# Kernel optimization log

Hardware: AMD Instinct MI355X
Metric: run time of the kernel (lower is better)

Reference implementation:

```python
import jax, jax.numpy as jnp
import numpy as np

N_NODES = 200000
N_EDGES = 4000000  # doubled (w2b + b2w), matches edge_weight param size
N_W2B = 2000000


def gcn_conv(x, W, b, src, dst, ew, n):
    # PyG GCNConv with add_self_loops=True, symmetric normalization.
    loop = jnp.arange(n)
    src_sl = jnp.concatenate([src, loop])
    dst_sl = jnp.concatenate([dst, loop])
    w_sl = jnp.concatenate([ew, jnp.ones((n,), ew.dtype)])  # self-loop weight 1
    deg = jax.ops.segment_sum(w_sl, dst_sl, num_segments=n)
    dinv = jnp.where(deg > 0, jax.lax.rsqrt(deg), 0.0)
    norm = dinv[src_sl] * w_sl * dinv[dst_sl]          # [E+N]
    xw = x @ W                                          # [N, out]
    msg = xw[src_sl] * norm[:, None]                    # [E+N, out]
    out = jax.ops.segment_sum(msg, dst_sl, num_segments=n)
    return out + b


def setup_inputs() -> dict:
    key = jax.random.key(0)
    ks = jax.random.split(key, 16)
    h1, h2, h3, h4, out = 8, 16, 32, 4, 3
    inp = 7

    def lin_init(k, fan_in, fan_out):
        bound = 1.0 / np.sqrt(fan_in)
        kw, kb = jax.random.split(k)
        W = jax.random.uniform(kw, (fan_in, fan_out), jnp.float32, -bound, bound)
        b = jax.random.uniform(kb, (fan_out,), jnp.float32, -bound, bound)
        return W, b

    x = jax.random.normal(ks[0], (N_NODES, inp), jnp.float32)
    edge_index = jax.random.randint(ks[1], (2, N_EDGES), 0, N_NODES, jnp.int64)
    w2b = jax.random.randint(ks[2], (2, N_W2B), 0, N_NODES, jnp.int64)
    edge_weight = jnp.ones((N_EDGES,), jnp.float32)  # Parameter init: ones

    W1, b1 = lin_init(ks[3], inp, h1)
    W2, b2 = lin_init(ks[4], h1, h2)
    W3, b3 = lin_init(ks[5], h2, h3)
    Wl1, bl1 = lin_init(ks[6], 2 * h3, h4)
    Wl2, bl2 = lin_init(ks[7], h4, out)

    return dict(x=x, edge_index=edge_index, w2b=w2b, edge_weight=edge_weight,
                W1=W1, b1=b1, W2=W2, b2=b2, W3=W3, b3=b3,
                Wl1=Wl1, bl1=bl1, Wl2=Wl2, bl2=bl2)


def reference(x, edge_index, w2b, edge_weight,
              W1, b1, W2, b2, W3, b3, Wl1, bl1, Wl2, bl2):
    n = x.shape[0]
    src, dst = edge_index[0], edge_index[1]
    ew = jax.nn.sigmoid(edge_weight)
    h = jax.nn.relu(gcn_conv(x, W1, b1, src, dst, ew, n))
    h = jax.nn.relu(gcn_conv(h, W2, b2, src, dst, ew, n))
    h = jax.nn.relu(gcn_conv(h, W3, b3, src, dst, ew, n))
    # fused gather-concat replacing the per-edge python loop
    concat = jnp.concatenate([h[w2b[0]], h[w2b[1]]], axis=-1)  # [E_w2b, 2*h3]
    hidden = concat @ Wl1 + bl1
    edge_pred = hidden @ Wl2 + bl2
    return edge_pred
```

## Files before the change

kernel.cpp:

```cpp
#include <hip/hip_runtime.h>
#include <hip/hip_bf16.h>
#include <hip/hip_fp16.h>


#define NB1 768
#define NPB 256
#define MAXBINS 1024
#define TILE 4096
#define QS 16384.0f
#define QINV (1.0f / 16384.0f)

typedef _Float16 h2 __attribute__((ext_vector_type(2)));
typedef _Float16 h4 __attribute__((ext_vector_type(4)));
typedef _Float16 h8 __attribute__((ext_vector_type(8)));

__device__ __forceinline__ float sigmoidf_(float x) {
    return 1.0f / (1.0f + __expf(-x));
}

__global__ void p1a_hist(const int* __restrict__ dst, int* __restrict__ bh,
                         int ne, int nbins, int chunk) {
    __shared__ int h[MAXBINS];
    for (int k = threadIdx.x; k < nbins; k += 256) h[k] = 0;
    __syncthreads();
    int base = blockIdx.x * chunk;
    int end = min(base + chunk, ne);
    for (int e = base + threadIdx.x; e < end; e += 256)
        atomicAdd(&h[dst[e] >> 8], 1);
    __syncthreads();
    for (int k = threadIdx.x; k < nbins; k += 256)
        bh[(size_t)k * NB1 + blockIdx.x] = h[k];
}

__global__ void s1_scan(int* __restrict__ bh, int* __restrict__ bintot) {
    __shared__ int sums[256];
    constexpr int W = NB1 / 256;
    int* row = bh + (size_t)blockIdx.x * NB1;
    int v[W];
    int s = 0;
#pragma unroll
    for (int j = 0; j < W; ++j) { v[j] = row[threadIdx.x * W + j]; s += v[j]; }
    sums[threadIdx.x] = s;
    __syncthreads();
    for (int o = 1; o < 256; o <<= 1) {
        int t = (threadIdx.x >= o) ? sums[threadIdx.x - o] : 0;
        __syncthreads();
        sums[threadIdx.x] += t;
        __syncthreads();
    }
    int excl = sums[threadIdx.x] - s;
#pragma unroll
    for (int j = 0; j < W; ++j) { row[threadIdx.x * W + j] = excl; excl += v[j]; }
    if (threadIdx.x == 255) bintot[blockIdx.x] = sums[255];
}

__global__ void s2_scan(const int* __restrict__ bintot, int* __restrict__ binbase,
                        int nbins, int ne) {
    __shared__ int tmp[1024];
    int tid = threadIdx.x;
    int v = (tid < nbins) ? bintot[tid] : 0;
    tmp[tid] = v;
    __syncthreads();
    for (int o = 1; o < 1024; o <<= 1) {
        int t = (tid >= o) ? tmp[tid - o] : 0;
        __syncthreads();
        tmp[tid] += t;
        __syncthreads();
    }
    if (tid < nbins) binbase[tid] = tmp[tid] - v;
    if (tid == 0) binbase[nbins] = ne;
}

__global__ void p1b_scatter(const int* __restrict__ src, const int* __restrict__ dst,
                            const float* __restrict__ ew, const int* __restrict__ bh,
                            const int* __restrict__ binbase,
                            unsigned* __restrict__ edlo, unsigned char* __restrict__ eddl,
                            int ne, int nbins, int chunk) {
    __shared__ unsigned slo[TILE];
    __shared__ unsigned shi[TILE];
    __shared__ int hist[MAXBINS];
    __shared__ int boff[MAXBINS];
    __shared__ int cur[MAXBINS];
    __shared__ int wsum[4];
    int tid = threadIdx.x;
    int lane = tid & 63, wid = tid >> 6;
    for (int k = tid; k < nbins; k += 256)
        cur[k] = binbase[k] + bh[(size_t)k * NB1 + blockIdx.x];
    int base = blockIdx.x * chunk;
    int endb = min(base + chunk, ne);
    for (int t0 = base; t0 < endb; t0 += TILE) {
        int cnt = min(TILE, endb - t0);
        for (int k = tid; k < nbins; k += 256) hist[k] = 0;
        __syncthreads();
        for (int j = tid; j < cnt; j += 256)
            atomicAdd(&hist[dst[t0 + j] >> 8], 1);
        __syncthreads();
        int w0 = tid * 4;
        int lv[4];
        int ls = 0;
#pragma unroll
        for (int j = 0; j < 4; ++j) {
            lv[j] = (w0 + j < nbins) ? hist[w0 + j] : 0;
            ls += lv[j];
        }
        int s = ls;
        for (int o = 1; o < 64; o <<= 1) {
            int t = __shfl_up(s, o, 64);
            if (lane >= o) s += t;
        }
        if (lane == 63) wsum[wid] = s;
        __syncthreads();
        int wpre = 0;
        for (int w = 0; w < wid; ++w) wpre += wsum[w];
        int excl = wpre + s - ls;
#pragma unroll
        for (int j = 0; j < 4; ++j) {
            if (w0 + j < nbins) { boff[w0 + j] = excl; excl += lv[j]; }
        }
        __syncthreads();
        for (int j = tid; j < cnt; j += 256) {
            int e = t0 + j;
            int d = dst[e];
            int b = d >> 8;
            float w = sigmoidf_(ew[e]);
            int q = (int)fminf(w * QS + 0.5f, 16383.0f);
            unsigned lo = (unsigned)src[e] | ((unsigned)q << 18);
            int p = atomicAdd(&boff[b], 1);
            slo[p] = lo;
            shi[p] = ((unsigned)b << 8) | (unsigned)(d & 255);
        }
        __syncthreads();
        for (int j = tid; j < cnt; j += 256) {
            unsigned hv = shi[j];
            int b = (int)(hv >> 8);
            int g = cur[b] + (j - (boff[b] - hist[b]));
            edlo[g] = slo[j];
            eddl[g] = (unsigned char)(hv & 255u);
        }
        __syncthreads();
        for (int k = tid; k < nbins; k += 256) cur[k] += hist[k];
        __syncthreads();
    }
}

__global__ void p2_build(const unsigned* __restrict__ edlo, const unsigned char* __restrict__ eddl,
                         const int* __restrict__ binbase, unsigned* __restrict__ edata,
                         int* __restrict__ C, float* __restrict__ dinv,
                         const float* __restrict__ x, const float* __restrict__ W1,
                         _Float16* __restrict__ g0, int n, int ne, int nbins) {
    __shared__ int cnt[NPB];
    __shared__ int curs[NPB];
    __shared__ unsigned qsum[NPB];
    __shared__ float Ws[56];
    __shared__ int wsum[4];
    if (threadIdx.x < 56) Ws[threadIdx.x] = W1[threadIdx.x];
    int b = blockIdx.x;
    int E0 = binbase[b], E1 = binbase[b + 1];
    int tid = threadIdx.x;
    int lane = tid & 63, wid = tid >> 6;
    cnt[tid] = 0;
    qsum[tid] = 0;
    __syncthreads();
    for (int k = E0 + tid; k < E1; k += 256)
        atomicAdd(&cnt[(int)eddl[k]], 1);
    __syncthreads();
    int v = cnt[tid];
    int s = v;
    for (int o = 1; o < 64; o <<= 1) {
        int t = __shfl_up(s, o, 64);
        if (lane >= o) s += t;
    }
    if (lane == 63) wsum[wid] = s;
    __syncthreads();
    int wpre = 0;
    for (int w = 0; w < wid; ++w) wpre += wsum[w];
    int excl = wpre + s - v;
    curs[tid] = E0 + excl;
    int node = b * NPB + tid;
    if (node < n) C[node] = E0 + excl;
    if (b == 0 && tid == 0) C[n] = ne;
    __syncthreads();
    for (int k = E0 + tid; k < E1; k += 256) {
        unsigned lo = edlo[k];
        int dl = (int)eddl[k];
        int pos = atomicAdd(&curs[dl], 1);
        edata[pos] = lo;
        atomicAdd(&qsum[dl], lo >> 18);
    }
    __syncthreads();
    if (node < n) {
        float dv = rsqrtf((float)qsum[tid] * QINV + 1.0f);
        dinv[node] = dv;
        float xi[7];
#pragma unroll
        for (int k = 0; k < 7; ++k) xi[k] = x[(size_t)node * 7 + k];
        h8 r;
#pragma unroll
        for (int o = 0; o < 8; ++o) {
            float acc = 0.0f;
#pragma unroll
            for (int k = 0; k < 7; ++k) acc = fmaf(xi[k], Ws[k * 8 + o], acc);
            r[o] = (_Float16)(acc * dv);
        }
        *reinterpret_cast<h8*>(g0 + (size_t)node * 8) = r;
    }
}

__global__ void gather1_kernel(const _Float16* __restrict__ g, const float* __restrict__ dinv,
                               const int* __restrict__ C, const unsigned* __restrict__ edata,
                               const float* __restrict__ b1, _Float16* __restrict__ out, int n) {
    __shared__ float bs[8];
    if (threadIdx.x < 8) bs[threadIdx.x] = b1[threadIdx.x];
    __syncthreads();
    long long t = (long long)blockIdx.x * blockDim.x + threadIdx.x;
    int i = (int)(t >> 3);
    int l8 = (int)(t & 7);
    if (i >= n) return;
    int beg = C[i], end = C[i + 1];
    float acc[8] = {0.f, 0.f, 0.f, 0.f, 0.f, 0.f, 0.f, 0.f};
    if (l8 == 0) {
        h8 r = *reinterpret_cast<const h8*>(g + (size_t)i * 8);
#pragma unroll
        for (int j = 0; j < 8; ++j) acc[j] = (float)r[j];
    }
    int k = beg + l8;
    for (; k + 8 < end; k += 16) {
        unsigned v0 = edata[k];
        unsigned v1 = edata[k + 8];
        h8 r0 = *reinterpret_cast<const h8*>(g + (size_t)(v0 & 0x3FFFFu) * 8);
        h8 r1 = *reinterpret_cast<const h8*>(g + (size_t)(v1 & 0x3FFFFu) * 8);
        float w0 = (float)(v0 >> 18) * QINV;
        float w1 = (float)(v1 >> 18) * QINV;
#pragma unroll
        for (int j = 0; j < 8; ++j) acc[j] = fmaf((float)r0[j], w0, acc[j]);
#pragma unroll
        for (int j = 0; j < 8; ++j) acc[j] = fmaf((float)r1[j], w1, acc[j]);
    }
    if (k < end) {
        unsigned v = edata[k];
        float w = (float)(v >> 18) * QINV;
        h8 r = *reinterpret_cast<const h8*>(g + (size_t)(v & 0x3FFFFu) * 8);
#pragma unroll
        for (int j = 0; j < 8; ++j) acc[j] = fmaf((float)r[j], w, acc[j]);
    }
    bool t4 = (l8 & 4) != 0, t2 = (l8 & 2) != 0, t1 = (l8 & 1) != 0;
    float s4[4];
#pragma unroll
    for (int j = 0; j < 4; ++j) {
        float keep = t4 ? acc[4 + j] : acc[j];
        float send = t4 ? acc[j] : acc[4 + j];
        s4[j] = keep + __shfl_xor(send, 4, 64);
    }
    float s2[2];
#pragma unroll
    for (int j = 0; j < 2; ++j) {
        float keep = t2 ? s4[2 + j] : s4[j];
        float send = t2 ? s4[j] : s4[2 + j];
        s2[j] = keep + __shfl_xor(send, 2, 64);
    }
    float keep = t1 ? s2[1] : s2[0];
    float send = t1 ? s2[0] : s2[1];
    float s = keep + __shfl_xor(send, 1, 64);
    float dv = dinv[i];
    out[(size_t)i * 8 + l8] = (_Float16)(dv * fmaxf(dv * s + bs[l8], 0.0f));
}

__global__ void gather2_kernel(const _Float16* __restrict__ g, const float* __restrict__ dinv,
                               const int* __restrict__ C, const unsigned* __restrict__ edata,
                               const float* __restrict__ W2, const float* __restrict__ b2,
                               _Float16* __restrict__ out, int n) {
    __shared__ float Ws[128];
    __shared__ float bs[16];
    if (threadIdx.x < 128) Ws[threadIdx.x] = W2[threadIdx.x];
    if (threadIdx.x < 16) bs[threadIdx.x] = b2[threadIdx.x];
    __syncthreads();
    long long t = (long long)blockIdx.x * blockDim.x + threadIdx.x;
    int i = (int)(t >> 3);
    int l8 = (int)(t & 7);
    if (i >= n) return;
    int beg = C[i], end = C[i + 1];
    float acc[8] = {0.f, 0.f, 0.f, 0.f, 0.f, 0.f, 0.f, 0.f};
    if (l8 == 0) {
        h8 r = *reinterpret_cast<const h8*>(g + (size_t)i * 8);
#pragma unroll
        for (int j = 0; j < 8; ++j) acc[j] = (float)r[j];
    }
    int k = beg + l8;
    for (; k + 8 < end; k += 16) {
        unsigned v0 = edata[k];
        unsigned v1 = edata[k + 8];
        h8 r0 = *reinterpret_cast<const h8*>(g + (size_t)(v0 & 0x3FFFFu) * 8);
        h8 r1 = *reinterpret_cast<const h8*>(g + (size_t)(v1 & 0x3FFFFu) * 8);
        float w0 = (float)(v0 >> 18) * QINV;
        float w1 = (float)(v1 >> 18) * QINV;
#pragma unroll
        for (int j = 0; j < 8; ++j) acc[j] = fmaf((float)r0[j], w0, acc[j]);
#pragma unroll
        for (int j = 0; j < 8; ++j) acc[j] = fmaf((float)r1[j], w1, acc[j]);
    }
    if (k < end) {
        unsigned v = edata[k];
        float w = (float)(v >> 18) * QINV;
        h8 r = *reinterpret_cast<const h8*>(g + (size_t)(v & 0x3FFFFu) * 8);
#pragma unroll
        for (int j = 0; j < 8; ++j) acc[j] = fmaf((float)r[j], w, acc[j]);
    }
#pragma unroll
    for (int j = 0; j < 8; ++j) {
        acc[j] += __shfl_xor(acc[j], 1, 64);
        acc[j] += __shfl_xor(acc[j], 2, 64);
        acc[j] += __shfl_xor(acc[j], 4, 64);
    }
    float dv = dinv[i];
    float raw[8];
#pragma unroll
    for (int j = 0; j < 8; ++j) raw[j] = acc[j] * dv;
    int o0 = l8 * 2;
    h2 o2;
#pragma unroll
    for (int jo = 0; jo < 2; ++jo) {
        int o = o0 + jo;
        float h = bs[o];
#pragma unroll
        for (int k2 = 0; k2 < 8; ++k2) h = fmaf(raw[k2], Ws[k2 * 16 + o], h);
        o2[jo] = (_Float16)(dv * fmaxf(h, 0.0f));
    }
    *reinterpret_cast<h2*>(out + (size_t)i * 16 + o0) = o2;
}

__global__ void gather3_kernel(const _Float16* __restrict__ g, const float* __restrict__ dinv,
                               const int* __restrict__ C, const unsigned* __restrict__ edata,
                               _Float16* __restrict__ raw3, int n) {
    long long t = (long long)blockIdx.x * blockDim.x + threadIdx.x;
    int i = (int)(t >> 3);
    int l8 = (int)(t & 7);
    if (i >= n) return;
    int beg = C[i], end = C[i + 1];
    float acc[16];
#pragma unroll
    for (int j = 0; j < 16; ++j) acc[j] = 0.0f;
    if (l8 == 0) {
        h8 r0 = *reinterpret_cast<const h8*>(g + (size_t)i * 16);
        h8 r1 = *reinterpret_cast<const h8*>(g + (size_t)i * 16 + 8);
#pragma unroll
        for (int j = 0; j < 8; ++j) { acc[j] = (float)r0[j]; acc[8 + j] = (float)r1[j]; }
    }
    int k = beg + l8;
    for (; k + 8 < end; k += 16) {
        unsigned v0 = edata[k];
        unsigned v1 = edata[k + 8];
        size_t i0 = (size_t)(v0 & 0x3FFFFu) * 16;
        size_t i1 = (size_t)(v1 & 0x3FFFFu) * 16;
        h8 a0 = *reinterpret_cast<const h8*>(g + i0);
        h8 a1 = *reinterpret_cast<const h8*>(g + i0 + 8);
        h8 c0 = *reinterpret_cast<const h8*>(g + i1);
        h8 c1 = *reinterpret_cast<const h8*>(g + i1 + 8);
        float w0 = (float)(v0 >> 18) * QINV;
        float w1 = (float)(v1 >> 18) * QINV;
#pragma unroll
        for (int j = 0; j < 8; ++j) acc[j] = fmaf((float)a0[j], w0, acc[j]);
#pragma unroll
        for (int j = 0; j < 8; ++j) acc[8 + j] = fmaf((float)a1[j], w0, acc[8 + j]);
#pragma unroll
        for (int j = 0; j < 8; ++j) acc[j] = fmaf((float)c0[j], w1, acc[j]);
#pragma unroll
        for (int j = 0; j < 8; ++j) acc[8 + j] = fmaf((float)c1[j], w1, acc[8 + j]);
    }
    if (k < end) {
        unsigned v = edata[k];
        size_t i0 = (size_t)(v & 0x3FFFFu) * 16;
        h8 a0 = *reinterpret_cast<const h8*>(g + i0);
        h8 a1 = *reinterpret_cast<const h8*>(g + i0 + 8);
        float w = (float)(v >> 18) * QINV;
#pragma unroll
        for (int j = 0; j < 8; ++j) acc[j] = fmaf((float)a0[j], w, acc[j]);
#pragma unroll
        for (int j = 0; j < 8; ++j) acc[8 + j] = fmaf((float)a1[j], w, acc[8 + j]);
    }
    bool t4 = (l8 & 4) != 0, t2 = (l8 & 2) != 0, t1 = (l8 & 1) != 0;
    float s8[8];
#pragma unroll
    for (int j = 0; j < 8; ++j) {
        float keep = t4 ? acc[8 + j] : acc[j];
        float send = t4 ? acc[j] : acc[8 + j];
        s8[j] = keep + __shfl_xor(send, 4, 64);
    }
    float s4[4];
#pragma unroll
    for (int j = 0; j < 4; ++j) {
        float keep = t2 ? s8[4 + j] : s8[j];
        float send = t2 ? s8[j] : s8[4 + j];
        s4[j] = keep + __shfl_xor(send, 2, 64);
    }
    float s2[2];
#pragma unroll
    for (int j = 0; j < 2; ++j) {
        float keep = t1 ? s4[2 + j] : s4[j];
        float send = t1 ? s4[j] : s4[2 + j];
        s2[j] = keep + __shfl_xor(send, 1, 64);
    }
    float dv = dinv[i];
    h2 o2;
    o2[0] = (_Float16)(s2[0] * dv);
    o2[1] = (_Float16)(s2[1] * dv);
    *reinterpret_cast<h2*>(raw3 + (size_t)i * 16 + l8 * 2) = o2;
}

__global__ void dense3_kernel(const _Float16* __restrict__ raw3,
                              const float* __restrict__ W3, const float* __restrict__ b3,
                              const float* __restrict__ Wl1, const float* __restrict__ bl1,
                              const float* __restrict__ Wl2, const float* __restrict__ bl2,
                              _Float16* __restrict__ pqh, int n) {
    __shared__ __align__(16) float WsT[512];
    __shared__ float bs[32];
    __shared__ float wfs[192];
    __shared__ float bfs[3];
    for (int t = threadIdx.x; t < 512; t += 256) {
        int k = t >> 5, o = t & 31;
        WsT[o * 16 + k] = W3[t];
    }
    if (threadIdx.x < 32) bs[threadIdx.x] = b3[threadIdx.x];
    if (threadIdx.x < 192) {
        int f = threadIdx.x / 3, j = threadIdx.x % 3;
        float a = 0.0f;
#pragma unroll
        for (int k = 0; k < 4; ++k) a = fmaf(Wl1[f * 4 + k], Wl2[k * 3 + j], a);
        wfs[threadIdx.x] = a;
    }
    if (threadIdx.x < 3) {
        float a = bl2[threadIdx.x];
#pragma unroll
        for (int k = 0; k < 4; ++k) a = fmaf(bl1[k], Wl2[k * 3 + threadIdx.x], a);
        bfs[threadIdx.x] = a;
    }
    __syncthreads();
    int i = blockIdx.x * 256 + threadIdx.x;
    if (i >= n) return;
    h8 r0 = *reinterpret_cast<const h8*>(raw3 + (size_t)i * 16);
    h8 r1 = *reinterpret_cast<const h8*>(raw3 + (size_t)i * 16 + 8);
    float raw[16];
#pragma unroll
    for (int j = 0; j < 8; ++j) { raw[j] = (float)r0[j]; raw[8 + j] = (float)r1[j]; }
    float p0 = bfs[0], p1 = bfs[1], p2 = bfs[2];
    float q0 = 0.0f, q1 = 0.0f, q2 = 0.0f;
#pragma unroll
    for (int o = 0; o < 32; ++o) {
        const float4* w4 = reinterpret_cast<const float4*>(WsT + o * 16);
        float4 wa = w4[0], wb = w4[1], wc = w4[2], wd = w4[3];
        float h = bs[o];
        h = fmaf(raw[0], wa.x, h);  h = fmaf(raw[1], wa.y, h);
        h = fmaf(raw[2], wa.z, h);  h = fmaf(raw[3], wa.w, h);
        h = fmaf(raw[4], wb.x, h);  h = fmaf(raw[5], wb.y, h);
        h = fmaf(raw[6], wb.z, h);  h = fmaf(raw[7], wb.w, h);
        h = fmaf(raw[8], wc.x, h);  h = fmaf(raw[9], wc.y, h);
        h = fmaf(raw[10], wc.z, h); h = fmaf(raw[11], wc.w, h);
        h = fmaf(raw[12], wd.x, h); h = fmaf(raw[13], wd.y, h);
        h = fmaf(raw[14], wd.z, h); h = fmaf(raw[15], wd.w, h);
        h = fmaxf(h, 0.0f);
        p0 = fmaf(h, wfs[o * 3 + 0], p0);
        p1 = fmaf(h, wfs[o * 3 + 1], p1);
        p2 = fmaf(h, wfs[o * 3 + 2], p2);
        q0 = fmaf(h, wfs[(32 + o) * 3 + 0], q0);
        q1 = fmaf(h, wfs[(32 + o) * 3 + 1], q1);
        q2 = fmaf(h, wfs[(32 + o) * 3 + 2], q2);
    }
    h8 o8;
    o8[0] = (_Float16)p0; o8[1] = (_Float16)p1; o8[2] = (_Float16)p2; o8[3] = (_Float16)0.0f;
    o8[4] = (_Float16)q0; o8[5] = (_Float16)q1; o8[6] = (_Float16)q2; o8[7] = (_Float16)0.0f;
    *reinterpret_cast<h8*>(pqh + (size_t)i * 8) = o8;
}

__global__ void head_kernel(const int* __restrict__ w2b, const _Float16* __restrict__ pqh,
                            float* __restrict__ out, int nw) {
    int e = blockIdx.x * blockDim.x + threadIdx.x;
    if (e >= nw) return;
    int a = w2b[e];
    int b = w2b[(size_t)nw + e];
    h4 P = *reinterpret_cast<const h4*>(pqh + (size_t)a * 8);
    h4 Q = *reinterpret_cast<const h4*>(pqh + (size_t)b * 8 + 4);
    out[(size_t)e * 3 + 0] = (float)P[0] + (float)Q[0];
    out[(size_t)e * 3 + 1] = (float)P[1] + (float)Q[1];
    out[(size_t)e * 3 + 2] = (float)P[2] + (float)Q[2];
}

extern "C" void kernel_launch(void* const* d_in, const int* in_sizes, int n_in,
                              void* d_out, int out_size, void* d_ws, size_t ws_size,
                              hipStream_t stream) {
    const float* x   = (const float*)d_in[0];
    const int* eidx  = (const int*)d_in[1];
    const int* w2b   = (const int*)d_in[2];
    const float* ew  = (const float*)d_in[3];
    const float* W1  = (const float*)d_in[4];
    const float* b1  = (const float*)d_in[5];
    const float* W2  = (const float*)d_in[6];
    const float* b2  = (const float*)d_in[7];
    const float* W3  = (const float*)d_in[8];
    const float* b3  = (const float*)d_in[9];
    const float* Wl1 = (const float*)d_in[10];
    const float* bl1 = (const float*)d_in[11];
    const float* Wl2 = (const float*)d_in[12];
    const float* bl2 = (const float*)d_in[13];
    float* out = (float*)d_out;

    const int n  = in_sizes[0] / 7;
    const int ne = in_sizes[1] / 2;
    const int nw = in_sizes[2] / 2;
    const int* src = eidx;
    const int* dst = eidx + ne;

    const int nbins = (n + NPB - 1) / NPB;
    const int chunk = (ne + NB1 - 1) / NB1;

    float*     ws      = (float*)d_ws;
    float*     dinv    = ws;
    int*       C       = (int*)(ws + n);
    unsigned*  edata   = (unsigned*)(ws + 2 * (size_t)n + 16);
    int*       bh      = (int*)(edata + ne);
    int*       bintot  = bh + (size_t)nbins * NB1;
    int*       binbase = bintot + MAXBINS;
    _Float16*  g0      = (_Float16*)(binbase + MAXBINS);
    float*     bregion = (float*)(g0 + (size_t)n * 8);
    unsigned*  edlo    = (unsigned*)bregion;
    unsigned char* eddl = (unsigned char*)(edlo + ne);
    _Float16*  g1      = (_Float16*)bregion;
    _Float16*  g2      = (_Float16*)(bregion + 4 * (size_t)n);
    _Float16*  pqh     = (_Float16*)(bregion + 12 * (size_t)n);
    _Float16*  raw3    = (_Float16*)(bregion + 16 * (size_t)n);

    const int Bl = 256;
    auto blks = [&](long long t) { return (int)((t + Bl - 1) / Bl); };
    const int nb8 = blks((long long)n * 8);

    p1a_hist<<<NB1, Bl, 0, stream>>>(dst, bh, ne, nbins, chunk);
    s1_scan<<<nbins, Bl, 0, stream>>>(bh, bintot);
    s2_scan<<<1, 1024, 0, stream>>>(bintot, binbase, nbins, ne);
    p1b_scatter<<<NB1, Bl, 0, stream>>>(src, dst, ew, bh, binbase, edlo, eddl, ne, nbins, chunk);
    p2_build<<<nbins, Bl, 0, stream>>>(edlo, eddl, binbase, edata, C, dinv, x, W1, g0, n, ne, nbins);

    gather1_kernel<<<nb8, Bl, 0, stream>>>(g0, dinv, C, edata, b1, g1, n);
    gather2_kernel<<<nb8, Bl, 0, stream>>>(g1, dinv, C, edata, W2, b2, g2, n);
    gather3_kernel<<<nb8, Bl, 0, stream>>>(g2, dinv, C, edata, raw3, n);
    dense3_kernel<<<blks(n), Bl, 0, stream>>>(raw3, W3, b3, Wl1, bl1, Wl2, bl2, pqh, n);

    head_kernel<<<blks(nw), Bl, 0, stream>>>(w2b, pqh, out, nw);
}
```

Before: 365.0 us.

## Replace binned two-pass CSR sort with global-atomic degree count and scatter

```diff
diff --git a/kernel.cpp b/kernel.cpp
--- a/kernel.cpp
+++ b/kernel.cpp
@@ -3,10 +3,8 @@
 #include <hip/hip_fp16.h>
 
 
-#define NB1 768
 #define NPB 256
 #define MAXBINS 1024
-#define TILE 4096
 #define QS 16384.0f
 #define QINV (1.0f / 16384.0f)
 
@@ -18,40 +16,25 @@
     return 1.0f / (1.0f + __expf(-x));
 }
 
-__global__ void p1a_hist(const int* __restrict__ dst, int* __restrict__ bh,
-                         int ne, int nbins, int chunk) {
-    __shared__ int h[MAXBINS];
-    for (int k = threadIdx.x; k < nbins; k += 256) h[k] = 0;
-    __syncthreads();
-    int base = blockIdx.x * chunk;
-    int end = min(base + chunk, ne);
-    for (int e = base + threadIdx.x; e < end; e += 256)
-        atomicAdd(&h[dst[e] >> 8], 1);
-    __syncthreads();
-    for (int k = threadIdx.x; k < nbins; k += 256)
-        bh[(size_t)k * NB1 + blockIdx.x] = h[k];
-}
-
-__global__ void s1_scan(int* __restrict__ bh, int* __restrict__ bintot) {
-    __shared__ int sums[256];
-    constexpr int W = NB1 / 256;
-    int* row = bh + (size_t)blockIdx.x * NB1;
-    int v[W];
-    int s = 0;
-#pragma unroll
-    for (int j = 0; j < W; ++j) { v[j] = row[threadIdx.x * W + j]; s += v[j]; }
-    sums[threadIdx.x] = s;
-    __syncthreads();
-    for (int o = 1; o < 256; o <<= 1) {
-        int t = (threadIdx.x >= o) ? sums[threadIdx.x - o] : 0;
-        __syncthreads();
-        sums[threadIdx.x] += t;
-        __syncthreads();
-    }
-    int excl = sums[threadIdx.x] - s;
-#pragma unroll
-    for (int j = 0; j < W; ++j) { row[threadIdx.x * W + j] = excl; excl += v[j]; }
-    if (threadIdx.x == 255) bintot[blockIdx.x] = sums[255];
+__global__ void zero_kernel(int* __restrict__ p, int nwords) {
+    int i = blockIdx.x * 256 + threadIdx.x;
+    if (i < nwords) p[i] = 0;
+}
+
+__global__ void d1_degree(const int* __restrict__ dst, int* __restrict__ deg, int ne) {
+    int e = blockIdx.x * 256 + threadIdx.x;
+    if (e < ne) atomicAdd(&deg[dst[e]], 1);
+}
+
+__global__ void d2a_sums(const int* __restrict__ deg, int* __restrict__ bintot, int n) {
+    __shared__ int wsum[4];
+    int tid = threadIdx.x, lane = tid & 63, wid = tid >> 6;
+    int node = blockIdx.x * NPB + tid;
+    int v = (node < n) ? deg[node] : 0;
+    for (int o = 1; o < 64; o <<= 1) v += __shfl_xor(v, o, 64);
+    if (lane == 0) wsum[wid] = v;
+    __syncthreads();
+    if (tid == 0) bintot[blockIdx.x] = wsum[0] + wsum[1] + wsum[2] + wsum[3];
 }
 
 __global__ void s2_scan(const int* __restrict__ bintot, int* __restrict__ binbase,
@@ -71,100 +54,13 @@
     if (tid == 0) binbase[nbins] = ne;
 }
 
-__global__ void p1b_scatter(const int* __restrict__ src, const int* __restrict__ dst,
-                            const float* __restrict__ ew, const int* __restrict__ bh,
-                            const int* __restrict__ binbase,
-                            unsigned* __restrict__ edlo, unsigned char* __restrict__ eddl,
-                            int ne, int nbins, int chunk) {
-    __shared__ unsigned slo[TILE];
-    __shared__ unsigned shi[TILE];
-    __shared__ int hist[MAXBINS];
-    __shared__ int boff[MAXBINS];
-    __shared__ int cur[MAXBINS];
+__global__ void d2b_offsets(const int* __restrict__ deg, const int* __restrict__ binbase,
+                            int* __restrict__ C, int* __restrict__ cur, int n, int ne) {
     __shared__ int wsum[4];
-    int tid = threadIdx.x;
-    int lane = tid & 63, wid = tid >> 6;
-    for (int k = tid; k < nbins; k += 256)
-        cur[k] = binbase[k] + bh[(size_t)k * NB1 + blockIdx.x];
-    int base = blockIdx.x * chunk;
-    int endb = min(base + chunk, ne);
-    for (int t0 = base; t0 < endb; t0 += TILE) {
-        int cnt = min(TILE, endb - t0);
-        for (int k = tid; k < nbins; k += 256) hist[k] = 0;
-        __syncthreads();
-        for (int j = tid; j < cnt; j += 256)
-            atomicAdd(&hist[dst[t0 + j] >> 8], 1);
-        __syncthreads();
-        int w0 = tid * 4;
-        int lv[4];
-        int ls = 0;
-#pragma unroll
-        for (int j = 0; j < 4; ++j) {
-            lv[j] = (w0 + j < nbins) ? hist[w0 + j] : 0;
-            ls += lv[j];
-        }
-        int s = ls;
-        for (int o = 1; o < 64; o <<= 1) {
-            int t = __shfl_up(s, o, 64);
-            if (lane >= o) s += t;
-        }
-        if (lane == 63) wsum[wid] = s;
-        __syncthreads();
-        int wpre = 0;
-        for (int w = 0; w < wid; ++w) wpre += wsum[w];
-        int excl = wpre + s - ls;
-#pragma unroll
-        for (int j = 0; j < 4; ++j) {
-            if (w0 + j < nbins) { boff[w0 + j] = excl; excl += lv[j]; }
-        }
-        __syncthreads();
-        for (int j = tid; j < cnt; j += 256) {
-            int e = t0 + j;
-            int d = dst[e];
-            int b = d >> 8;
-            float w = sigmoidf_(ew[e]);
-            int q = (int)fminf(w * QS + 0.5f, 16383.0f);
-            unsigned lo = (unsigned)src[e] | ((unsigned)q << 18);
-            int p = atomicAdd(&boff[b], 1);
-            slo[p] = lo;
-            shi[p] = ((unsigned)b << 8) | (unsigned)(d & 255);
-        }
-        __syncthreads();
-        for (int j = tid; j < cnt; j += 256) {
-            unsigned hv = shi[j];
-            int b = (int)(hv >> 8);
-            int g = cur[b] + (j - (boff[b] - hist[b]));
-            edlo[g] = slo[j];
-            eddl[g] = (unsigned char)(hv & 255u);
-        }
-        __syncthreads();
-        for (int k = tid; k < nbins; k += 256) cur[k] += hist[k];
-        __syncthreads();
-    }
-}
-
-__global__ void p2_build(const unsigned* __restrict__ edlo, const unsigned char* __restrict__ eddl,
-                         const int* __restrict__ binbase, unsigned* __restrict__ edata,
-                         int* __restrict__ C, float* __restrict__ dinv,
-                         const float* __restrict__ x, const float* __restrict__ W1,
-                         _Float16* __restrict__ g0, int n, int ne, int nbins) {
-    __shared__ int cnt[NPB];
-    __shared__ int curs[NPB];
-    __shared__ unsigned qsum[NPB];
-    __shared__ float Ws[56];
-    __shared__ int wsum[4];
-    if (threadIdx.x < 56) Ws[threadIdx.x] = W1[threadIdx.x];
+    int tid = threadIdx.x, lane = tid & 63, wid = tid >> 6;
     int b = blockIdx.x;
-    int E0 = binbase[b], E1 = binbase[b + 1];
-    int tid = threadIdx.x;
-    int lane = tid & 63, wid = tid >> 6;
-    cnt[tid] = 0;
-    qsum[tid] = 0;
-    __syncthreads();
-    for (int k = E0 + tid; k < E1; k += 256)
-        atomicAdd(&cnt[(int)eddl[k]], 1);
-    __syncthreads();
-    int v = cnt[tid];
+    int node = b * NPB + tid;
+    int v = (node < n) ? deg[node] : 0;
     int s = v;
     for (int o = 1; o < 64; o <<= 1) {
         int t = __shfl_up(s, o, 64);
@@ -174,36 +70,47 @@
     __syncthreads();
     int wpre = 0;
     for (int w = 0; w < wid; ++w) wpre += wsum[w];
-    int excl = wpre + s - v;
-    curs[tid] = E0 + excl;
-    int node = b * NPB + tid;
-    if (node < n) C[node] = E0 + excl;
+    int excl = binbase[b] + wpre + s - v;
+    if (node < n) { C[node] = excl; cur[node] = excl; }
     if (b == 0 && tid == 0) C[n] = ne;
-    __syncthreads();
-    for (int k = E0 + tid; k < E1; k += 256) {
-        unsigned lo = edlo[k];
-        int dl = (int)eddl[k];
-        int pos = atomicAdd(&curs[dl], 1);
-        edata[pos] = lo;
-        atomicAdd(&qsum[dl], lo >> 18);
-    }
-    __syncthreads();
-    if (node < n) {
-        float dv = rsqrtf((float)qsum[tid] * QINV + 1.0f);
-        dinv[node] = dv;
-        float xi[7];
-#pragma unroll
-        for (int k = 0; k < 7; ++k) xi[k] = x[(size_t)node * 7 + k];
-        h8 r;
-#pragma unroll
-        for (int o = 0; o < 8; ++o) {
-            float acc = 0.0f;
-#pragma unroll
-            for (int k = 0; k < 7; ++k) acc = fmaf(xi[k], Ws[k * 8 + o], acc);
-            r[o] = (_Float16)(acc * dv);
-        }
-        *reinterpret_cast<h8*>(g0 + (size_t)node * 8) = r;
-    }
+}
+
+__global__ void d3_scatter(const int* __restrict__ src, const int* __restrict__ dst,
+                           const float* __restrict__ ew, int* __restrict__ cur,
+                           int* __restrict__ qsumI, unsigned* __restrict__ edata, int ne) {
+    int e = blockIdx.x * 256 + threadIdx.x;
+    if (e >= ne) return;
+    int d = dst[e];
+    float w = sigmoidf_(ew[e]);
+    int q = (int)fminf(w * QS + 0.5f, 16383.0f);
+    unsigned lo = (unsigned)src[e] | ((unsigned)q << 18);
+    int pos = atomicAdd(&cur[d], 1);
+    atomicAdd(&qsumI[d], q);
+    edata[pos] = lo;
+}
+
+__global__ void d4_g0(const int* __restrict__ qsumI, const float* __restrict__ x,
+                      const float* __restrict__ W1, float* __restrict__ dinv,
+                      _Float16* __restrict__ g0, int n) {
+    __shared__ float Ws[56];
+    if (threadIdx.x < 56) Ws[threadIdx.x] = W1[threadIdx.x];
+    __syncthreads();
+    int i = blockIdx.x * 256 + threadIdx.x;
+    if (i >= n) return;
+    float dv = rsqrtf((float)qsumI[i] * QINV + 1.0f);
+    dinv[i] = dv;
+    float xi[7];
+#pragma unroll
+    for (int k = 0; k < 7; ++k) xi[k] = x[(size_t)i * 7 + k];
+    h8 r;
+#pragma unroll
+    for (int o = 0; o < 8; ++o) {
+        float acc = 0.0f;
+#pragma unroll
+        for (int k = 0; k < 7; ++k) acc = fmaf(xi[k], Ws[k * 8 + o], acc);
+        r[o] = (_Float16)(acc * dv);
+    }
+    *reinterpret_cast<h8*>(g0 + (size_t)i * 8) = r;
 }
 
 __global__ void gather1_kernel(const _Float16* __restrict__ g, const float* __restrict__ dinv,
@@ -509,19 +416,18 @@
     const int* dst = eidx + ne;
 
     const int nbins = (n + NPB - 1) / NPB;
-    const int chunk = (ne + NB1 - 1) / NB1;
 
     float*     ws      = (float*)d_ws;
     float*     dinv    = ws;
     int*       C       = (int*)(ws + n);
     unsigned*  edata   = (unsigned*)(ws + 2 * (size_t)n + 16);
-    int*       bh      = (int*)(edata + ne);
-    int*       bintot  = bh + (size_t)nbins * NB1;
+    int*       deg     = (int*)(edata + ne);
+    int*       qsumI   = deg + n;
+    int*       cur     = qsumI + n;
+    int*       bintot  = cur + n;
     int*       binbase = bintot + MAXBINS;
-    _Float16*  g0      = (_Float16*)(binbase + MAXBINS);
+    _Float16*  g0      = (_Float16*)(binbase + MAXBINS + 16);
     float*     bregion = (float*)(g0 + (size_t)n * 8);
-    unsigned*  edlo    = (unsigned*)bregion;
-    unsigned char* eddl = (unsigned char*)(edlo + ne);
     _Float16*  g1      = (_Float16*)bregion;
     _Float16*  g2      = (_Float16*)(bregion + 4 * (size_t)n);
     _Float16*  pqh     = (_Float16*)(bregion + 12 * (size_t)n);
@@ -531,11 +437,13 @@
     auto blks = [&](long long t) { return (int)((t + Bl - 1) / Bl); };
     const int nb8 = blks((long long)n * 8);
 
-    p1a_hist<<<NB1, Bl, 0, stream>>>(dst, bh, ne, nbins, chunk);
-    s1_scan<<<nbins, Bl, 0, stream>>>(bh, bintot);
+    zero_kernel<<<blks(2 * (long long)n), Bl, 0, stream>>>(deg, 2 * n);
+    d1_degree<<<blks(ne), Bl, 0, stream>>>(dst, deg, ne);
+    d2a_sums<<<nbins, Bl, 0, stream>>>(deg, bintot, n);
     s2_scan<<<1, 1024, 0, stream>>>(bintot, binbase, nbins, ne);
-    p1b_scatter<<<NB1, Bl, 0, stream>>>(src, dst, ew, bh, binbase, edlo, eddl, ne, nbins, chunk);
-    p2_build<<<nbins, Bl, 0, stream>>>(edlo, eddl, binbase, edata, C, dinv, x, W1, g0, n, ne, nbins);
+    d2b_offsets<<<nbins, Bl, 0, stream>>>(deg, binbase, C, cur, n, ne);
+    d3_scatter<<<blks(ne), Bl, 0, stream>>>(src, dst, ew, cur, qsumI, edata, ne);
+    d4_g0<<<blks(n), Bl, 0, stream>>>(qsumI, x, W1, dinv, g0, n);
 
     gather1_kernel<<<nb8, Bl, 0, stream>>>(g0, dinv, C, edata, b1, g1, n);
     gather2_kernel<<<nb8, Bl, 0, stream>>>(g1, dinv, C, edata, W2, b2, g2, n);
```

New measurement: 800.9 us. 2.19x slower.

## Pack scatter entries into 64-bit words and split layer-3 gather into halves

Applied to the files above, without the earlier changes.

```diff
diff --git a/kernel.cpp b/kernel.cpp
--- a/kernel.cpp
+++ b/kernel.cpp
@@ -74,14 +74,14 @@
 __global__ void p1b_scatter(const int* __restrict__ src, const int* __restrict__ dst,
                             const float* __restrict__ ew, const int* __restrict__ bh,
                             const int* __restrict__ binbase,
-                            unsigned* __restrict__ edlo, unsigned char* __restrict__ eddl,
+                            unsigned long long* __restrict__ b64,
                             int ne, int nbins, int chunk) {
-    __shared__ unsigned slo[TILE];
-    __shared__ unsigned shi[TILE];
+    __shared__ unsigned long long stage[TILE];
     __shared__ int hist[MAXBINS];
     __shared__ int boff[MAXBINS];
     __shared__ int cur[MAXBINS];
     __shared__ int wsum[4];
+    constexpr int MPT = TILE / 256;
     int tid = threadIdx.x;
     int lane = tid & 63, wid = tid >> 6;
     for (int k = tid; k < nbins; k += 256)
@@ -92,8 +92,19 @@
         int cnt = min(TILE, endb - t0);
         for (int k = tid; k < nbins; k += 256) hist[k] = 0;
         __syncthreads();
-        for (int j = tid; j < cnt; j += 256)
-            atomicAdd(&hist[dst[t0 + j] >> 8], 1);
+        unsigned long long ent[MPT];
+        int m = 0;
+        for (int j = tid; j < cnt; j += 256) {
+            int e = t0 + j;
+            int d = dst[e];
+            float w = sigmoidf_(ew[e]);
+            int q = (int)fminf(w * QS + 0.5f, 16383.0f);
+            int b = d >> 8;
+            ent[m++] = (unsigned long long)((unsigned)src[e] | ((unsigned)q << 18))
+                     | ((unsigned long long)(d & 255) << 32)
+                     | ((unsigned long long)b << 40);
+            atomicAdd(&hist[b], 1);
+        }
         __syncthreads();
         int w0 = tid * 4;
         int lv[4];
@@ -118,24 +129,16 @@
             if (w0 + j < nbins) { boff[w0 + j] = excl; excl += lv[j]; }
         }
         __syncthreads();
+        for (int j = 0; j < m; ++j) {
+            int b = (int)(ent[j] >> 40);
+            int p = atomicAdd(&boff[b], 1);
+            stage[p] = ent[j];
+        }
+        __syncthreads();
         for (int j = tid; j < cnt; j += 256) {
-            int e = t0 + j;
-            int d = dst[e];
-            int b = d >> 8;
-            float w = sigmoidf_(ew[e]);
-            int q = (int)fminf(w * QS + 0.5f, 16383.0f);
-            unsigned lo = (unsigned)src[e] | ((unsigned)q << 18);
-            int p = atomicAdd(&boff[b], 1);
-            slo[p] = lo;
-            shi[p] = ((unsigned)b << 8) | (unsigned)(d & 255);
-        }
-        __syncthreads();
-        for (int j = tid; j < cnt; j += 256) {
-            unsigned hv = shi[j];
-            int b = (int)(hv >> 8);
-            int g = cur[b] + (j - (boff[b] - hist[b]));
-            edlo[g] = slo[j];
-            eddl[g] = (unsigned char)(hv & 255u);
+            unsigned long long v = stage[j];
+            int b = (int)(v >> 40);
+            b64[cur[b] + (j - (boff[b] - hist[b]))] = v;
         }
         __syncthreads();
         for (int k = tid; k < nbins; k += 256) cur[k] += hist[k];
@@ -143,7 +146,7 @@
     }
 }
 
-__global__ void p2_build(const unsigned* __restrict__ edlo, const unsigned char* __restrict__ eddl,
+__global__ void p2_build(const unsigned long long* __restrict__ b64,
                          const int* __restrict__ binbase, unsigned* __restrict__ edata,
                          int* __restrict__ C, float* __restrict__ dinv,
                          const float* __restrict__ x, const float* __restrict__ W1,
@@ -162,7 +165,7 @@
     qsum[tid] = 0;
     __syncthreads();
     for (int k = E0 + tid; k < E1; k += 256)
-        atomicAdd(&cnt[(int)eddl[k]], 1);
+        atomicAdd(&cnt[(int)((b64[k] >> 32) & 0xFF)], 1);
     __syncthreads();
     int v = cnt[tid];
     int s = v;
@@ -181,11 +184,11 @@
     if (b == 0 && tid == 0) C[n] = ne;
     __syncthreads();
     for (int k = E0 + tid; k < E1; k += 256) {
-        unsigned lo = edlo[k];
-        int dl = (int)eddl[k];
+        unsigned long long e64 = b64[k];
+        int dl = (int)((e64 >> 32) & 0xFF);
         int pos = atomicAdd(&curs[dl], 1);
-        edata[pos] = lo;
-        atomicAdd(&qsum[dl], lo >> 18);
+        edata[pos] = (unsigned)(e64 & 0xFFFFFFFFu);
+        atomicAdd(&qsum[dl], (unsigned)((e64 >> 18) & 0x3FFFu));
     }
     __syncthreads();
     if (node < n) {
@@ -268,7 +271,7 @@
 __global__ void gather2_kernel(const _Float16* __restrict__ g, const float* __restrict__ dinv,
                                const int* __restrict__ C, const unsigned* __restrict__ edata,
                                const float* __restrict__ W2, const float* __restrict__ b2,
-                               _Float16* __restrict__ out, int n) {
+                               _Float16* __restrict__ g2lo, _Float16* __restrict__ g2hi, int n) {
     __shared__ float Ws[128];
     __shared__ float bs[16];
     if (threadIdx.x < 128) Ws[threadIdx.x] = W2[threadIdx.x];
@@ -325,88 +328,68 @@
         for (int k2 = 0; k2 < 8; ++k2) h = fmaf(raw[k2], Ws[k2 * 16 + o], h);
         o2[jo] = (_Float16)(dv * fmaxf(h, 0.0f));
     }
-    *reinterpret_cast<h2*>(out + (size_t)i * 16 + o0) = o2;
-}
-
-__global__ void gather3_kernel(const _Float16* __restrict__ g, const float* __restrict__ dinv,
-                               const int* __restrict__ C, const unsigned* __restrict__ edata,
-                               _Float16* __restrict__ raw3, int n) {
+    _Float16* basep = (l8 < 4) ? g2lo : g2hi;
+    int oo = (l8 < 4) ? o0 : (o0 - 8);
+    *reinterpret_cast<h2*>(basep + (size_t)i * 8 + oo) = o2;
+}
+
+__global__ void gather3h_kernel(const _Float16* __restrict__ g, const float* __restrict__ dinv,
+                                const int* __restrict__ C, const unsigned* __restrict__ edata,
+                                _Float16* __restrict__ rout, int n) {
     long long t = (long long)blockIdx.x * blockDim.x + threadIdx.x;
     int i = (int)(t >> 3);
     int l8 = (int)(t & 7);
     if (i >= n) return;
     int beg = C[i], end = C[i + 1];
-    float acc[16];
-#pragma unroll
-    for (int j = 0; j < 16; ++j) acc[j] = 0.0f;
+    float acc[8] = {0.f, 0.f, 0.f, 0.f, 0.f, 0.f, 0.f, 0.f};
     if (l8 == 0) {
-        h8 r0 = *reinterpret_cast<const h8*>(g + (size_t)i * 16);
-        h8 r1 = *reinterpret_cast<const h8*>(g + (size_t)i * 16 + 8);
-#pragma unroll
-        for (int j = 0; j < 8; ++j) { acc[j] = (float)r0[j]; acc[8 + j] = (float)r1[j]; }
+        h8 r = *reinterpret_cast<const h8*>(g + (size_t)i * 8);
+#pragma unroll
+        for (int j = 0; j < 8; ++j) acc[j] = (float)r[j];
     }
     int k = beg + l8;
     for (; k + 8 < end; k += 16) {
         unsigned v0 = edata[k];
         unsigned v1 = edata[k + 8];
-        size_t i0 = (size_t)(v0 & 0x3FFFFu) * 16;
-        size_t i1 = (size_t)(v1 & 0x3FFFFu) * 16;
-        h8 a0 = *reinterpret_cast<const h8*>(g + i0);
-        h8 a1 = *reinterpret_cast<const h8*>(g + i0 + 8);
-        h8 c0 = *reinterpret_cast<const h8*>(g + i1);
-        h8 c1 = *reinterpret_cast<const h8*>(g + i1 + 8);
+        h8 r0 = *reinterpret_cast<const h8*>(g + (size_t)(v0 & 0x3FFFFu) * 8);
+        h8 r1 = *reinterpret_cast<const h8*>(g + (size_t)(v1 & 0x3FFFFu) * 8);
         float w0 = (float)(v0 >> 18) * QINV;
         float w1 = (float)(v1 >> 18) * QINV;
 #pragma unroll
-        for (int j = 0; j < 8; ++j) acc[j] = fmaf((float)a0[j], w0, acc[j]);
-#pragma unroll
-        for (int j = 0; j < 8; ++j) acc[8 + j] = fmaf((float)a1[j], w0, acc[8 + j]);
-#pragma unroll
-        for (int j = 0; j < 8; ++j) acc[j] = fmaf((float)c0[j], w1, acc[j]);
-#pragma unroll
-        for (int j = 0; j < 8; ++j) acc[8 + j] = fmaf((float)c1[j], w1, acc[8 + j]);
+        for (int j = 0; j < 8; ++j) acc[j] = fmaf((float)r0[j], w0, acc[j]);
+#pragma unroll
+        for (int j = 0; j < 8; ++j) acc[j] = fmaf((float)r1[j], w1, acc[j]);
     }
     if (k < end) {
         unsigned v = edata[k];
-        size_t i0 = (size_t)(v & 0x3FFFFu) * 16;
-        h8 a0 = *reinterpret_cast<const h8*>(g + i0);
-        h8 a1 = *reinterpret_cast<const h8*>(g + i0 + 8);
         float w = (float)(v >> 18) * QINV;
-#pragma unroll
-        for (int j = 0; j < 8; ++j) acc[j] = fmaf((float)a0[j], w, acc[j]);
-#pragma unroll
-        for (int j = 0; j < 8; ++j) acc[8 + j] = fmaf((float)a1[j], w, acc[8 + j]);
+        h8 r = *reinterpret_cast<const h8*>(g + (size_t)(v & 0x3FFFFu) * 8);
+#pragma unroll
+        for (int j = 0; j < 8; ++j) acc[j] = fmaf((float)r[j], w, acc[j]);
     }
     bool t4 = (l8 & 4) != 0, t2 = (l8 & 2) != 0, t1 = (l8 & 1) != 0;
-    float s8[8];
-#pragma unroll
-    for (int j = 0; j < 8; ++j) {
-        float keep = t4 ? acc[8 + j] : acc[j];
-        float send = t4 ? acc[j] : acc[8 + j];
-        s8[j] = keep + __shfl_xor(send, 4, 64);
-    }
     float s4[4];
 #pragma unroll
     for (int j = 0; j < 4; ++j) {
-        float keep = t2 ? s8[4 + j] : s8[j];
-        float send = t2 ? s8[j] : s8[4 + j];
-        s4[j] = keep + __shfl_xor(send, 2, 64);
+        float keep = t4 ? acc[4 + j] : acc[j];
+        float send = t4 ? acc[j] : acc[4 + j];
+        s4[j] = keep + __shfl_xor(send, 4, 64);
     }
     float s2[2];
 #pragma unroll
     for (int j = 0; j < 2; ++j) {
-        float keep = t1 ? s4[2 + j] : s4[j];
-        float send = t1 ? s4[j] : s4[2 + j];
-        s2[j] = keep + __shfl_xor(send, 1, 64);
-    }
-    float dv = dinv[i];
-    h2 o2;
-    o2[0] = (_Float16)(s2[0] * dv);
-    o2[1] = (_Float16)(s2[1] * dv);
-    *reinterpret_cast<h2*>(raw3 + (size_t)i * 16 + l8 * 2) = o2;
-}
-
-__global__ void dense3_kernel(const _Float16* __restrict__ raw3,
+        float keep = t2 ? s4[2 + j] : s4[j];
+        float send = t2 ? s4[j] : s4[2 + j];
+        s2[j] = keep + __shfl_xor(send, 2, 64);
+    }
+    float keep = t1 ? s2[1] : s2[0];
+    float send = t1 ? s2[0] : s2[1];
+    float s = keep + __shfl_xor(send, 1, 64);
+    rout[(size_t)i * 8 + l8] = (_Float16)(s * dinv[i]);
+}
+
+__global__ void dense3_kernel(const _Float16* __restrict__ raw3lo,
+                              const _Float16* __restrict__ raw3hi,
                               const float* __restrict__ W3, const float* __restrict__ b3,
                               const float* __restrict__ Wl1, const float* __restrict__ bl1,
                               const float* __restrict__ Wl2, const float* __restrict__ bl2,
@@ -436,8 +419,8 @@
     __syncthreads();
     int i = blockIdx.x * 256 + threadIdx.x;
     if (i >= n) return;
-    h8 r0 = *reinterpret_cast<const h8*>(raw3 + (size_t)i * 16);
-    h8 r1 = *reinterpret_cast<const h8*>(raw3 + (size_t)i * 16 + 8);
+    h8 r0 = *reinterpret_cast<const h8*>(raw3lo + (size_t)i * 8);
+    h8 r1 = *reinterpret_cast<const h8*>(raw3hi + (size_t)i * 8);
     float raw[16];
 #pragma unroll
     for (int j = 0; j < 8; ++j) { raw[j] = (float)r0[j]; raw[8 + j] = (float)r1[j]; }
@@ -520,12 +503,13 @@
     int*       binbase = bintot + MAXBINS;
     _Float16*  g0      = (_Float16*)(binbase + MAXBINS);
     float*     bregion = (float*)(g0 + (size_t)n * 8);
-    unsigned*  edlo    = (unsigned*)bregion;
-    unsigned char* eddl = (unsigned char*)(edlo + ne);
+    unsigned long long* b64 = (unsigned long long*)bregion;
     _Float16*  g1      = (_Float16*)bregion;
-    _Float16*  g2      = (_Float16*)(bregion + 4 * (size_t)n);
+    _Float16*  g2lo    = (_Float16*)(bregion + 4 * (size_t)n);
+    _Float16*  g2hi    = (_Float16*)(bregion + 8 * (size_t)n);
     _Float16*  pqh     = (_Float16*)(bregion + 12 * (size_t)n);
-    _Float16*  raw3    = (_Float16*)(bregion + 16 * (size_t)n);
+    _Float16*  raw3lo  = (_Float16*)(bregion + 16 * (size_t)n);
+    _Float16*  raw3hi  = (_Float16*)(bregion + 20 * (size_t)n);
 
     const int Bl = 256;
     auto blks = [&](long long t) { return (int)((t + Bl - 1) / Bl); };
@@ -534,13 +518,14 @@
     p1a_hist<<<NB1, Bl, 0, stream>>>(dst, bh, ne, nbins, chunk);
     s1_scan<<<nbins, Bl, 0, stream>>>(bh, bintot);
     s2_scan<<<1, 1024, 0, stream>>>(bintot, binbase, nbins, ne);
-    p1b_scatter<<<NB1, Bl, 0, stream>>>(src, dst, ew, bh, binbase, edlo, eddl, ne, nbins, chunk);
-    p2_build<<<nbins, Bl, 0, stream>>>(edlo, eddl, binbase, edata, C, dinv, x, W1, g0, n, ne, nbins);
+    p1b_scatter<<<NB1, Bl, 0, stream>>>(src, dst, ew, bh, binbase, b64, ne, nbins, chunk);
+    p2_build<<<nbins, Bl, 0, stream>>>(b64, binbase, edata, C, dinv, x, W1, g0, n, ne, nbins);
 
     gather1_kernel<<<nb8, Bl, 0, stream>>>(g0, dinv, C, edata, b1, g1, n);
-    gather2_kernel<<<nb8, Bl, 0, stream>>>(g1, dinv, C, edata, W2, b2, g2, n);
-    gather3_kernel<<<nb8, Bl, 0, stream>>>(g2, dinv, C, edata, raw3, n);
-    dense3_kernel<<<blks(n), Bl, 0, stream>>>(raw3, W3, b3, Wl1, bl1, Wl2, bl2, pqh, n);
+    gather2_kernel<<<nb8, Bl, 0, stream>>>(g1, dinv, C, edata, W2, b2, g2lo, g2hi, n);
+    gather3h_kernel<<<nb8, Bl, 0, stream>>>(g2lo, dinv, C, edata, raw3lo, n);
+    gather3h_kernel<<<nb8, Bl, 0, stream>>>(g2hi, dinv, C, edata, raw3hi, n);
+    dense3_kernel<<<blks(n), Bl, 0, stream>>>(raw3lo, raw3hi, W3, b3, Wl1, bl1, Wl2, bl2, pqh, n);
 
     head_kernel<<<blks(nw), Bl, 0, stream>>>(w2b, pqh, out, nw);
 }
```

Measured after the change: 359.2 us. About the same (-1.6%).
